# Kernel tuning notes

Hardware: AMD Instinct MI355X
Metric: run time of the kernel (lower is better)

## Reference

```python
import jax, jax.numpy as jnp
import numpy as np

EMBED_DIM = 1024
NUM_HEADS = 16
HEAD_DIM = EMBED_DIM // NUM_HEADS
BSZ, TGT, SRC = 4, 2048, 2048


def setup_inputs() -> dict:
    key = jax.random.key(0)
    ks = jax.random.split(key, 8)
    s = EMBED_DIM ** -0.5  # keep activations O(1)
    return {
        "query": jax.random.normal(ks[0], (BSZ, TGT, EMBED_DIM), jnp.float32),
        "key": jax.random.normal(ks[1], (BSZ, SRC, EMBED_DIM), jnp.float32),
        "key_padding_mask": jnp.ones((BSZ, SRC), jnp.float32),
        "Wq": jax.random.normal(ks[2], (EMBED_DIM, EMBED_DIM), jnp.float32) * s,
        "bq": jnp.zeros((EMBED_DIM,), jnp.float32),
        "Wk": jax.random.normal(ks[3], (EMBED_DIM, EMBED_DIM), jnp.float32) * s,
        "bk": jnp.zeros((EMBED_DIM,), jnp.float32),
        "Wv": jax.random.normal(ks[4], (EMBED_DIM, EMBED_DIM), jnp.float32) * s,
        "bv": jnp.zeros((EMBED_DIM,), jnp.float32),
        "Wo": jax.random.normal(ks[5], (EMBED_DIM, EMBED_DIM), jnp.float32) * s,
        "bo": jnp.zeros((EMBED_DIM,), jnp.float32),
    }


def _split_heads(x, bsz, seqlen):
    # [b, s, e] -> [b, h, s, d]
    return x.reshape(bsz, seqlen, NUM_HEADS, HEAD_DIM).transpose(0, 2, 1, 3)


def reference(query, key, key_padding_mask, Wq, bq, Wk, bk, Wv, bv, Wo, bo):
    bsz, src_len, embed_dim = key.shape
    tgt_len = query.shape[1]
    scaling = HEAD_DIM ** -0.5

    q = (query @ Wq.T + bq) * scaling                # [b, t, e]
    k = key @ Wk.T + bk                              # [b, s, e]
    v = key @ Wv.T + bv                              # [b, s, e]

    qh = _split_heads(q, bsz, tgt_len)               # [b, h, t, d]
    kh = _split_heads(k, bsz, src_len)               # [b, h, s, d]
    vh = _split_heads(v, bsz, src_len)               # [b, h, s, d]

    scores = jnp.einsum('bhtd,bhsd->bhts', qh, kh)   # [b, h, t, s]

    # _expand_mask: additive mask, 0 where mask==1, finfo.min where mask==0
    inv = 1.0 - key_padding_mask.astype(scores.dtype)
    neg = jnp.finfo(scores.dtype).min
    add_mask = jnp.where(inv.astype(bool), neg, inv)  # [b, s]
    scores = scores + add_mask[:, None, None, :]

    probs = jax.nn.softmax(scores, axis=-1)          # dropout p=0 / eval -> identity

    out = jnp.einsum('bhts,bhsd->bhtd', probs, vh)   # [b, h, t, d]
    out = out.transpose(0, 2, 1, 3).reshape(bsz, tgt_len, embed_dim)
    return out @ Wo.T + bo
```

## Files before the change

kernel.cpp:

```cpp
#include <hip/hip_runtime.h>

typedef unsigned short u16;
typedef __attribute__((ext_vector_type(8))) short bf16x8;
typedef __attribute__((ext_vector_type(4))) float f32x4;
typedef __attribute__((ext_vector_type(16))) float f32x16;

#define LOG2E 1.44269504088896f

__device__ inline u16 f2b(float f) {
  union { float f; unsigned u; } x; x.f = f;
  unsigned r = x.u + 0x7fffu + ((x.u >> 16) & 1u);
  return (u16)(r >> 16);
}

__device__ inline void gload_lds16(const void* g, void* l) {
  __builtin_amdgcn_global_load_lds(
      (__attribute__((address_space(1))) void*)(g),
      (__attribute__((address_space(3))) void*)(l), 16, 0, 0);
}

__device__ inline unsigned cvtpk_bf16(float lo, float hi_) {
  unsigned r;
  asm("v_cvt_pk_bf16_f32 %0, %1, %2" : "=v"(r) : "v"(lo), "v"(hi_));
  return r;
}
__device__ inline float exp2_hw(float x) { return __builtin_amdgcn_exp2f(x); }

__global__ __launch_bounds__(256) void cvt_all(
    const float* __restrict__ q, const float* __restrict__ k,
    const float* __restrict__ wq, const float* __restrict__ wk,
    const float* __restrict__ wv, const float* __restrict__ wo,
    u16* __restrict__ qb, u16* __restrict__ kb,
    u16* __restrict__ wqb, u16* __restrict__ wkb,
    u16* __restrict__ wvb, u16* __restrict__ wob) {
  int b = blockIdx.x;
  const float* in;
  u16* out;
  if (b < 8192) {
    in = q; out = qb;
  } else if (b < 16384) {
    in = k; out = kb; b -= 8192;
  } else {
    const int w = (b - 16384) >> 10;
    b = (b - 16384) & 1023;
    in = (w == 0) ? wq : (w == 1) ? wk : (w == 2) ? wv : wo;
    out = (w == 0) ? wqb : (w == 1) ? wkb : (w == 2) ? wvb : wob;
  }
  const int i = b * 256 + threadIdx.x;
  const float4 v = ((const float4*)in)[i];
  union { u16 s[4]; uint2 u; } o;
  o.s[0] = f2b(v.x); o.s[1] = f2b(v.y); o.s[2] = f2b(v.z); o.s[3] = f2b(v.w);
  ((uint2*)out)[i] = o.u;
}


__global__ __launch_bounds__(256) void gemm_o(
    const u16* __restrict__ A, const u16* __restrict__ W,
    const float* __restrict__ bias, float* __restrict__ Cout,
    int K) {
  __shared__ __align__(16) u16 lA[2][128 * 64];
  __shared__ __align__(16) u16 lW[2][128 * 64];
  const int tid = threadIdx.x, lane = tid & 63, wid = tid >> 6;
  const int wr = wid >> 1, wc = wid & 1;
  const int fr = lane & 15, fq = lane >> 4;
  const size_t abase = (size_t)blockIdx.x * 128 * K;
  const size_t wbase = (size_t)blockIdx.y * 128 * K;

  f32x4 acc[4][4];
#pragma unroll
  for (int i = 0; i < 4; ++i)
#pragma unroll
    for (int j = 0; j < 4; ++j) acc[i][j] = (f32x4){0.f, 0.f, 0.f, 0.f};

#define GSTAGE(bufi, kt)                                                          \
  do {                                                                            \
    _Pragma("unroll")                                                             \
    for (int is = 0; is < 4; ++is) {                                              \
      const int c = is * 256 + tid;                                               \
      const int r = c >> 3, ch = (c & 7) ^ (r & 7);                               \
      gload_lds16(A + abase + (size_t)r * K + (kt) + ch * 8, lA[bufi] + c * 8);   \
      gload_lds16(W + wbase + (size_t)r * K + (kt) + ch * 8, lW[bufi] + c * 8);   \
    }                                                                             \
  } while (0)

  GSTAGE(0, 0);
  __syncthreads();

  int buf = 0;
  for (int kt = 0; kt < K; kt += 64) {
    if (kt + 64 < K) GSTAGE(buf ^ 1, kt + 64);
#pragma unroll
    for (int kk = 0; kk < 2; ++kk) {
      bf16x8 af[4], wf[4];
#pragma unroll
      for (int m = 0; m < 4; ++m) {
        const int row = wr * 64 + m * 16 + fr;
        af[m] = *(const bf16x8*)&lA[buf][row * 64 + (((kk * 4 + fq) ^ (row & 7)) << 3)];
      }
#pragma unroll
      for (int n = 0; n < 4; ++n) {
        const int row = wc * 64 + n * 16 + fr;
        wf[n] = *(const bf16x8*)&lW[buf][row * 64 + (((kk * 4 + fq) ^ (row & 7)) << 3)];
      }
#pragma unroll
      for (int m = 0; m < 4; ++m)
#pragma unroll
        for (int n = 0; n < 4; ++n)
          acc[m][n] = __builtin_amdgcn_mfma_f32_16x16x32_bf16(af[m], wf[n], acc[m][n], 0, 0, 0);
    }
    __syncthreads();
    buf ^= 1;
  }
#undef GSTAGE

  const int row0 = blockIdx.x * 128 + wr * 64 + fq * 4;
  const int col0 = blockIdx.y * 128 + wc * 64 + fr;
#pragma unroll
  for (int n = 0; n < 4; ++n) {
    const int col = col0 + n * 16;
    const float bb = bias[col];
#pragma unroll
    for (int m = 0; m < 4; ++m) {
#pragma unroll
      for (int r = 0; r < 4; ++r) {
        const int row = row0 + m * 16 + r;
        Cout[(size_t)row * 1024 + col] = acc[m][n][r] + bb;
      }
    }
  }
}

__global__ __launch_bounds__(256) void gemm_qkv(
    const u16* __restrict__ qA, const u16* __restrict__ kA,
    const u16* __restrict__ Wq, const u16* __restrict__ Wk,
    const u16* __restrict__ Wv, const float* __restrict__ bq,
    const float* __restrict__ bk, const float* __restrict__ bv,
    u16* __restrict__ Qout, u16* __restrict__ Kout,
    u16* __restrict__ Vtout, int K) {
  __shared__ __align__(16) u16 lA[2][128 * 64];
  __shared__ __align__(16) u16 lW[2][128 * 64];
  const int tid = threadIdx.x, lane = tid & 63, wid = tid >> 6;
  const int wr = wid >> 1, wc = wid & 1;
  const int fr = lane & 15, fq = lane >> 4;
  const int path = blockIdx.y >> 3, ny = blockIdx.y & 7;
  const u16* A = (path == 0) ? qA : kA;
  const u16* W = (path == 0) ? Wq : (path == 1) ? Wk : Wv;
  const float* bias = (path == 0) ? bq : (path == 1) ? bk : bv;
  const size_t abase = (size_t)blockIdx.x * 128 * K;
  const size_t wbase = (size_t)ny * 128 * K;

  f32x4 acc[4][4];
#pragma unroll
  for (int i = 0; i < 4; ++i)
#pragma unroll
    for (int j = 0; j < 4; ++j) acc[i][j] = (f32x4){0.f, 0.f, 0.f, 0.f};

#define GSTAGE(bufi, kt)                                                          \
  do {                                                                            \
    _Pragma("unroll")                                                             \
    for (int is = 0; is < 4; ++is) {                                              \
      const int c = is * 256 + tid;                                               \
      const int r = c >> 3, ch = (c & 7) ^ (r & 7);                               \
      gload_lds16(A + abase + (size_t)r * K + (kt) + ch * 8, lA[bufi] + c * 8);   \
      gload_lds16(W + wbase + (size_t)r * K + (kt) + ch * 8, lW[bufi] + c * 8);   \
    }                                                                             \
  } while (0)

  GSTAGE(0, 0);
  __syncthreads();

  int buf = 0;
  for (int kt = 0; kt < K; kt += 64) {
    if (kt + 64 < K) GSTAGE(buf ^ 1, kt + 64);
#pragma unroll
    for (int kk = 0; kk < 2; ++kk) {
      bf16x8 af[4], wf[4];
#pragma unroll
      for (int m = 0; m < 4; ++m) {
        const int row = wr * 64 + m * 16 + fr;
        af[m] = *(const bf16x8*)&lA[buf][row * 64 + (((kk * 4 + fq) ^ (row & 7)) << 3)];
      }
#pragma unroll
      for (int n = 0; n < 4; ++n) {
        const int row = wc * 64 + n * 16 + fr;
        wf[n] = *(const bf16x8*)&lW[buf][row * 64 + (((kk * 4 + fq) ^ (row & 7)) << 3)];
      }
#pragma unroll
      for (int m = 0; m < 4; ++m)
#pragma unroll
        for (int n = 0; n < 4; ++n)
          acc[m][n] = __builtin_amdgcn_mfma_f32_16x16x32_bf16(af[m], wf[n], acc[m][n], 0, 0, 0);
    }
    __syncthreads();
    buf ^= 1;
  }
#undef GSTAGE

  if (path == 2) {
    const int bI = blockIdx.x >> 4;
    const int srow0 = ((blockIdx.x * 128) & 2047) + wr * 64 + fq * 4;
    const int col0 = ny * 128 + wc * 64 + fr;
#pragma unroll
    for (int n = 0; n < 4; ++n) {
      const int col = col0 + n * 16;
      const float bb = bias[col];
      const int h = col >> 6, dl = col & 63;
      u16* vrow = Vtout + ((size_t)((bI * 16 + h) * 64 + dl)) * 2048;
#pragma unroll
      for (int m = 0; m < 4; ++m) {
        const int s = srow0 + m * 16;
        const int x = s & 15;
        const int pos = (((s & 63) >> 4) * 2 + ((x >> 2) & 1)) * 8 + ((x & 3) | ((x & 8) >> 1));
        union { u16 s4[4]; uint2 u; } w;
#pragma unroll
        for (int r = 0; r < 4; ++r) w.s4[r] = f2b(acc[m][n][r] + bb);
        *(uint2*)&vrow[(s >> 6) * 64 + pos] = w.u;
      }
    }
  } else {
    const float alpha = (path == 0) ? 0.125f * LOG2E : 1.0f;
    u16* Cout = (path == 0) ? Qout : Kout;
    const int row0 = blockIdx.x * 128 + wr * 64 + fq * 4;
    const int col0 = ny * 128 + wc * 64 + fr;
#pragma unroll
    for (int n = 0; n < 4; ++n) {
      const int col = col0 + n * 16;
      const float bb = bias[col];
#pragma unroll
      for (int m = 0; m < 4; ++m) {
#pragma unroll
        for (int r = 0; r < 4; ++r) {
          const int row = row0 + m * 16 + r;
          Cout[(size_t)row * 1024 + col] = f2b((acc[m][n][r] + bb) * alpha);
        }
      }
    }
  }
}

__global__ __launch_bounds__(512, 3) void flash18(
    const u16* __restrict__ Qb, const u16* __restrict__ Kb,
    const u16* __restrict__ Vt, const float* __restrict__ mask,
    u16* __restrict__ Ob) {
  __shared__ __align__(16) u16 Kl[2][4096];
  __shared__ __align__(16) u16 Vl[2][4096];
  __shared__ unsigned long long bml[32];
  __shared__ float lbuf[8][32];

  const int f = blockIdx.x;
  const int xcd = f & 7, i = f >> 3;
  const int bh = xcd * 8 + (i >> 3);
  const int qt = i & 7;
  const int b = bh >> 4, h = bh & 15;
  const int tid = threadIdx.x, lane = tid & 63, wid = tid >> 6;
  const int l31 = lane & 31, hi = lane >> 5;
  const int qrow0 = qt * 256 + wid * 32;

  bf16x8 qf[4];
  {
    const u16* qp = Qb + ((size_t)(b * 2048 + qrow0 + l31)) * 1024 + h * 64;
#pragma unroll
    for (int dc = 0; dc < 4; ++dc) qf[dc] = *(const bf16x8*)(qp + dc * 16 + hi * 8);
  }

  const u16* kbase = Kb + ((size_t)(b * 2048)) * 1024 + h * 64;
  const u16* vbase = Vt + ((size_t)(bh * 64)) * 2048;
  const float* mrow = mask + b * 2048;

  const int l31s = tid & 31, his = (tid >> 5) & 1, mid = (tid >> 6) & 3,
            top = (tid >> 8) & 1;
  const int koff = (top * 32 + l31s) * 1024 + (mid * 2 + his) * 8;
  const int voff = (top * 32 + l31s) * 2048 + (mid * 2 + his) * 8;

  f32x16 o0 = {}, o1 = {};
  float l_r = 0.f;

#define STAGE(bufi, tt)                               \
  do {                                                \
    const u16* kb_t = kbase + (size_t)(tt) * 65536;   \
    const u16* vb_t = vbase + (tt) * 64;              \
    gload_lds16(kb_t + koff, &Kl[bufi][tid * 8]);     \
    gload_lds16(vb_t + voff, &Vl[bufi][tid * 8]);     \
  } while (0)

  STAGE(0, 0);

#pragma unroll
  for (int tt = 0; tt < 4; ++tt) {
    const int tile = wid * 4 + tt;
    const unsigned long long bmv = __ballot(mrow[tile * 64 + lane] == 1.0f);
    if (lane == 0) bml[tile] = bmv;
  }
  __syncthreads();

  const unsigned mflags =
      (unsigned)__ballot(lane < 32 && bml[lane] != ~0ull);

  for (int t = 0; t < 32; ++t) {
    const int cur = t & 1;
    if (t + 1 < 32) STAGE(cur ^ 1, t + 1);

    const u16* Kc = Kl[cur];
    const u16* Vc = Vl[cur];

#pragma unroll
    for (int n = 0; n < 2; ++n) {
      f32x16 acc = {};
#pragma unroll
      for (int dc = 0; dc < 4; ++dc) {
        const bf16x8 kf = *(const bf16x8*)&Kc[(n * 4 + dc) * 512 + lane * 8];
        acc = __builtin_amdgcn_mfma_f32_32x32x16_bf16(kf, qf[dc], acc, 0, 0, 0);
      }

#pragma unroll
      for (int reg = 0; reg < 16; ++reg) acc[reg] = exp2_hw(acc[reg]);

      if (mflags & (1u << t)) {
        const unsigned long long bm = bml[t];
#pragma unroll
        for (int reg = 0; reg < 16; ++reg) {
          const int k = n * 32 + (reg & 3) + 8 * (reg >> 2) + 4 * hi;
          if (!((bm >> k) & 1)) acc[reg] = 0.f;
        }
      }

      {
        float s0a = (acc[0] + acc[1]) + (acc[2] + acc[3]);
        float s1a = (acc[4] + acc[5]) + (acc[6] + acc[7]);
        float s2a = (acc[8] + acc[9]) + (acc[10] + acc[11]);
        float s3a = (acc[12] + acc[13]) + (acc[14] + acc[15]);
        l_r += (s0a + s1a) + (s2a + s3a);
      }

      bf16x8 pa0, pa1;
      {
        union { unsigned u[4]; bf16x8 v; } pk;
#pragma unroll
        for (int j = 0; j < 4; ++j) pk.u[j] = cvtpk_bf16(acc[2 * j], acc[2 * j + 1]);
        pa0 = pk.v;
#pragma unroll
        for (int j = 0; j < 4; ++j) pk.u[j] = cvtpk_bf16(acc[8 + 2 * j], acc[9 + 2 * j]);
        pa1 = pk.v;
      }

      {
        const bf16x8 v00 = *(const bf16x8*)&Vc[(0 * 4 + n * 2 + 0) * 512 + lane * 8];
        const bf16x8 v01 = *(const bf16x8*)&Vc[(0 * 4 + n * 2 + 1) * 512 + lane * 8];
        o0 = __builtin_amdgcn_mfma_f32_32x32x16_bf16(pa0, v00, o0, 0, 0, 0);
        o0 = __builtin_amdgcn_mfma_f32_32x32x16_bf16(pa1, v01, o0, 0, 0, 0);
      }
      {
        const bf16x8 v10 = *(const bf16x8*)&Vc[(1 * 4 + n * 2 + 0) * 512 + lane * 8];
        const bf16x8 v11 = *(const bf16x8*)&Vc[(1 * 4 + n * 2 + 1) * 512 + lane * 8];
        o1 = __builtin_amdgcn_mfma_f32_32x32x16_bf16(pa0, v10, o1, 0, 0, 0);
        o1 = __builtin_amdgcn_mfma_f32_32x32x16_bf16(pa1, v11, o1, 0, 0, 0);
      }
    }

    __syncthreads();
  }
#undef STAGE

  const float l_tot = l_r + __shfl_xor(l_r, 32);
  const float linv = 1.0f / l_tot;
  if (!hi) lbuf[wid][l31] = linv;
  __builtin_amdgcn_wave_barrier();
  float lv[16];
#pragma unroll
  for (int reg = 0; reg < 16; ++reg)
    lv[reg] = lbuf[wid][(reg & 3) + 8 * (reg >> 2) + 4 * hi];

  u16* ob = Ob + ((size_t)(b * 2048 + qrow0)) * 1024 + h * 64 + l31;
#pragma unroll
  for (int reg = 0; reg < 16; ++reg) {
    const int q = (reg & 3) + 8 * (reg >> 2) + 4 * hi;
    ob[(size_t)q * 1024] = f2b(o0[reg] * lv[reg]);
    ob[(size_t)q * 1024 + 32] = f2b(o1[reg] * lv[reg]);
  }
}

extern "C" void kernel_launch(void* const* d_in, const int* in_sizes, int n_in,
                              void* d_out, int out_size, void* d_ws, size_t ws_size,
                              hipStream_t stream) {
  const float* query = (const float*)d_in[0];
  const float* keyin = (const float*)d_in[1];
  const float* maskp = (const float*)d_in[2];
  const float* Wq = (const float*)d_in[3];
  const float* bq = (const float*)d_in[4];
  const float* Wk = (const float*)d_in[5];
  const float* bk = (const float*)d_in[6];
  const float* Wv = (const float*)d_in[7];
  const float* bv = (const float*)d_in[8];
  const float* Wo = (const float*)d_in[9];
  const float* bo = (const float*)d_in[10];

  char* ws = (char*)d_ws;
  const size_t ACT = (size_t)8192 * 1024 * 2;
  const size_t WMAT = (size_t)1024 * 1024 * 2;
  u16* qbf = (u16*)(ws);
  u16* kbf = (u16*)(ws + ACT);
  u16* wqb = (u16*)(ws + 2 * ACT);
  u16* wkb = (u16*)(ws + 2 * ACT + WMAT);
  u16* wvb = (u16*)(ws + 2 * ACT + 2 * WMAT);
  u16* wob = (u16*)(ws + 2 * ACT + 3 * WMAT);
  u16* Qb  = (u16*)(ws + 2 * ACT + 4 * WMAT);
  u16* Kb  = (u16*)(ws + 3 * ACT + 4 * WMAT);
  u16* VtDed = (u16*)(ws + 4 * ACT + 4 * WMAT);
  u16* attnb = kbf;

  cvt_all<<<20480, 256, 0, stream>>>(query, keyin, Wq, Wk, Wv, Wo,
                                     qbf, kbf, wqb, wkb, wvb, wob);

  gemm_qkv<<<dim3(64, 24), 256, 0, stream>>>(qbf, kbf, wqb, wkb, wvb,
                                             bq, bk, bv, Qb, Kb, VtDed, 1024);

  flash18<<<512, 512, 0, stream>>>(Qb, Kb, VtDed, maskp, attnb);

  gemm_o<<<dim3(64, 8), 256, 0, stream>>>(attnb, wob, bo, (float*)d_out, 1024);
}
```

Measured before the change: 179.9 us.

## Single-buffer LDS in projection GEMMs to raise occupancy to four blocks

Both projection GEMM kernels drop their double-buffered LDS tiles for a single buffer, which halves shared memory per block to 32 KB. Each k-step now loads its tile, syncs, then computes. Launch bounds ask for four blocks per CU. The aim is to hide load latency through more resident blocks instead of in-kernel prefetch, at the cost of losing overlap between global loads and MFMA inside a block.

Measured after the change: 169.8 us (median of 2 runs). 1.06x faster.

```diff
diff --git a/kernel.cpp b/kernel.cpp
--- a/kernel.cpp
+++ b/kernel.cpp
@@ -54,12 +54,12 @@
 }
 
 
-__global__ __launch_bounds__(256) void gemm_o(
+__global__ __launch_bounds__(256, 4) void gemm_o(
     const u16* __restrict__ A, const u16* __restrict__ W,
     const float* __restrict__ bias, float* __restrict__ Cout,
     int K) {
-  __shared__ __align__(16) u16 lA[2][128 * 64];
-  __shared__ __align__(16) u16 lW[2][128 * 64];
+  __shared__ __align__(16) u16 lA[128 * 64];
+  __shared__ __align__(16) u16 lW[128 * 64];
   const int tid = threadIdx.x, lane = tid & 63, wid = tid >> 6;
   const int wr = wid >> 1, wc = wid & 1;
   const int fr = lane & 15, fq = lane >> 4;
@@ -72,35 +72,32 @@
 #pragma unroll
     for (int j = 0; j < 4; ++j) acc[i][j] = (f32x4){0.f, 0.f, 0.f, 0.f};
 
-#define GSTAGE(bufi, kt)                                                          \
+#define GSTAGE(kt)                                                                \
   do {                                                                            \
     _Pragma("unroll")                                                             \
     for (int is = 0; is < 4; ++is) {                                              \
       const int c = is * 256 + tid;                                               \
       const int r = c >> 3, ch = (c & 7) ^ (r & 7);                               \
-      gload_lds16(A + abase + (size_t)r * K + (kt) + ch * 8, lA[bufi] + c * 8);   \
-      gload_lds16(W + wbase + (size_t)r * K + (kt) + ch * 8, lW[bufi] + c * 8);   \
+      gload_lds16(A + abase + (size_t)r * K + (kt) + ch * 8, lA + c * 8);         \
+      gload_lds16(W + wbase + (size_t)r * K + (kt) + ch * 8, lW + c * 8);         \
     }                                                                             \
   } while (0)
 
-  GSTAGE(0, 0);
-  __syncthreads();
-
-  int buf = 0;
   for (int kt = 0; kt < K; kt += 64) {
-    if (kt + 64 < K) GSTAGE(buf ^ 1, kt + 64);
+    GSTAGE(kt);
+    __syncthreads();
 #pragma unroll
     for (int kk = 0; kk < 2; ++kk) {
       bf16x8 af[4], wf[4];
 #pragma unroll
       for (int m = 0; m < 4; ++m) {
         const int row = wr * 64 + m * 16 + fr;
-        af[m] = *(const bf16x8*)&lA[buf][row * 64 + (((kk * 4 + fq) ^ (row & 7)) << 3)];
+        af[m] = *(const bf16x8*)&lA[row * 64 + (((kk * 4 + fq) ^ (row & 7)) << 3)];
       }
 #pragma unroll
       for (int n = 0; n < 4; ++n) {
         const int row = wc * 64 + n * 16 + fr;
-        wf[n] = *(const bf16x8*)&lW[buf][row * 64 + (((kk * 4 + fq) ^ (row & 7)) << 3)];
+        wf[n] = *(const bf16x8*)&lW[row * 64 + (((kk * 4 + fq) ^ (row & 7)) << 3)];
       }
 #pragma unroll
       for (int m = 0; m < 4; ++m)
@@ -109,7 +106,6 @@
           acc[m][n] = __builtin_amdgcn_mfma_f32_16x16x32_bf16(af[m], wf[n], acc[m][n], 0, 0, 0);
     }
     __syncthreads();
-    buf ^= 1;
   }
 #undef GSTAGE
 
@@ -130,15 +126,15 @@
   }
 }
 
-__global__ __launch_bounds__(256) void gemm_qkv(
+__global__ __launch_bounds__(256, 4) void gemm_qkv(
     const u16* __restrict__ qA, const u16* __restrict__ kA,
     const u16* __restrict__ Wq, const u16* __restrict__ Wk,
     const u16* __restrict__ Wv, const float* __restrict__ bq,
     const float* __restrict__ bk, const float* __restrict__ bv,
     u16* __restrict__ Qout, u16* __restrict__ Kout,
     u16* __restrict__ Vtout, int K) {
-  __shared__ __align__(16) u16 lA[2][128 * 64];
-  __shared__ __align__(16) u16 lW[2][128 * 64];
+  __shared__ __align__(16) u16 lA[128 * 64];
+  __shared__ __align__(16) u16 lW[128 * 64];
   const int tid = threadIdx.x, lane = tid & 63, wid = tid >> 6;
   const int wr = wid >> 1, wc = wid & 1;
   const int fr = lane & 15, fq = lane >> 4;
@@ -155,35 +151,32 @@
 #pragma unroll
     for (int j = 0; j < 4; ++j) acc[i][j] = (f32x4){0.f, 0.f, 0.f, 0.f};
 
-#define GSTAGE(bufi, kt)                                                          \
+#define GSTAGE(kt)                                                                \
   do {                                                                            \
     _Pragma("unroll")                                                             \
     for (int is = 0; is < 4; ++is) {                                              \
       const int c = is * 256 + tid;                                               \
       const int r = c >> 3, ch = (c & 7) ^ (r & 7);                               \
-      gload_lds16(A + abase + (size_t)r * K + (kt) + ch * 8, lA[bufi] + c * 8);   \
-      gload_lds16(W + wbase + (size_t)r * K + (kt) + ch * 8, lW[bufi] + c * 8);   \
+      gload_lds16(A + abase + (size_t)r * K + (kt) + ch * 8, lA + c * 8);         \
+      gload_lds16(W + wbase + (size_t)r * K + (kt) + ch * 8, lW + c * 8);         \
     }                                                                             \
   } while (0)
 
-  GSTAGE(0, 0);
-  __syncthreads();
-
-  int buf = 0;
   for (int kt = 0; kt < K; kt += 64) {
-    if (kt + 64 < K) GSTAGE(buf ^ 1, kt + 64);
+    GSTAGE(kt);
+    __syncthreads();
 #pragma unroll
     for (int kk = 0; kk < 2; ++kk) {
       bf16x8 af[4], wf[4];
 #pragma unroll
       for (int m = 0; m < 4; ++m) {
         const int row = wr * 64 + m * 16 + fr;
-        af[m] = *(const bf16x8*)&lA[buf][row * 64 + (((kk * 4 + fq) ^ (row & 7)) << 3)];
+        af[m] = *(const bf16x8*)&lA[row * 64 + (((kk * 4 + fq) ^ (row & 7)) << 3)];
       }
 #pragma unroll
       for (int n = 0; n < 4; ++n) {
         const int row = wc * 64 + n * 16 + fr;
-        wf[n] = *(const bf16x8*)&lW[buf][row * 64 + (((kk * 4 + fq) ^ (row & 7)) << 3)];
+        wf[n] = *(const bf16x8*)&lW[row * 64 + (((kk * 4 + fq) ^ (row & 7)) << 3)];
       }
 #pragma unroll
       for (int m = 0; m < 4; ++m)
@@ -192,7 +185,6 @@
           acc[m][n] = __builtin_amdgcn_mfma_f32_16x16x32_bf16(af[m], wf[n], acc[m][n], 0, 0, 0);
     }
     __syncthreads();
-    buf ^= 1;
   }
 #undef GSTAGE
 
```
